# Performance work log

Hardware: AMD Instinct MI355X
Metric: run time of the kernel (lower is better)

The kernel has to match this reference:

```python
import jax, jax.numpy as jnp
import numpy as np

B, TIN, TOUT = 64, 256, 400
NM, BF = 80, 512
MID, H, PRE = BF // 4, 2 * BF, BF // 2
LOC_F, LOC_K = 32, 31


def lstm_cell(x, h, c, Wih, Whh, bih, bhh):
    gates = x @ Wih.T + bih + h @ Whh.T + bhh
    i, f, g, o = jnp.split(gates, 4, axis=-1)
    c2 = jax.nn.sigmoid(f) * c + jax.nn.sigmoid(i) * jnp.tanh(g)
    h2 = jax.nn.sigmoid(o) * jnp.tanh(c2)
    return h2, c2


def setup_inputs() -> dict:
    key = jax.random.key(0)
    ks = jax.random.split(key, 24)
    def p(k, shape, fan_in):
        return jax.random.normal(k, shape, jnp.float32) / np.sqrt(fan_in)
    return {
        'input': jax.random.normal(ks[0], (B, TIN, BF), jnp.float32),
        'input_mask': jnp.ones((B, TIN), jnp.bool_),
        'target': jax.random.normal(ks[1], (B, NM, TOUT), jnp.float32),
        'W_pre1': p(ks[2], (PRE, NM), NM), 'b_pre1': jnp.zeros((PRE,), jnp.float32),
        'W_pre2': p(ks[3], (PRE, PRE), PRE), 'b_pre2': jnp.zeros((PRE,), jnp.float32),
        'Wq': p(ks[4], (MID, H), H),
        'Wk': p(ks[5], (MID, BF), BF),
        'loc_conv': p(ks[6], (LOC_F, 2, LOC_K), 2 * LOC_K),
        'Wloc': p(ks[7], (MID, LOC_F), LOC_F),
        'v_att': p(ks[8], (MID,), MID),
        'Wih1': p(ks[9], (4 * H, BF + PRE), BF + PRE), 'Whh1': p(ks[10], (4 * H, H), H),
        'bih1': jnp.zeros((4 * H,), jnp.float32), 'bhh1': jnp.zeros((4 * H,), jnp.float32),
        'Wih2': p(ks[11], (4 * H, BF + H), BF + H), 'Whh2': p(ks[12], (4 * H, H), H),
        'bih2': jnp.zeros((4 * H,), jnp.float32), 'bhh2': jnp.zeros((4 * H,), jnp.float32),
        'Wout': p(ks[13], (NM, BF + H), BF + H), 'bout': jnp.zeros((NM,), jnp.float32),
    }


def reference(input, input_mask, target, W_pre1, b_pre1, W_pre2, b_pre2, Wq, Wk,
              loc_conv, Wloc, v_att, Wih1, Whh1, bih1, bhh1, Wih2, Whh2, bih2, bhh2,
              Wout, bout):
    b, tin, f = input.shape
    nm, tout = target.shape[1], target.shape[2]
    # teacher-forcing shift: prepend zero frame, drop last
    tgt = jnp.concatenate([jnp.zeros((b, nm, 1), target.dtype), target[:, :, :-1]], 2)
    # PreNet: two 1x1 convs (== per-channel linears) + ReLU (dropout = eval identity)
    x = jax.nn.relu(jnp.einsum('bct,oc->bot', tgt, W_pre1) + b_pre1[None, :, None])
    x = jax.nn.relu(jnp.einsum('bct,oc->bot', x, W_pre2) + b_pre2[None, :, None])  # [B,PRE,Tout]
    key_proj = jnp.einsum('btf,mf->btm', input, Wk)  # [B,Tin,MID]
    pad = (LOC_K - 1) // 2

    def step(carry, xt):
        h1, c1, h2, c2, context, aw, awc = carry
        h1, c1 = lstm_cell(jnp.concatenate([xt, context], 1), h1, c1, Wih1, Whh1, bih1, bhh1)
        # location-sensitive attention
        wpair = jnp.stack([aw, awc], 1)  # [B,2,Tin]
        loc = jax.lax.conv_general_dilated(wpair, loc_conv, (1,), [(pad, pad)],
                                           dimension_numbers=('NCH', 'OIH', 'NCH'))
        loc_feat = jnp.einsum('bct,mc->btm', loc, Wloc)
        q = h1 @ Wq.T  # [B,MID]
        e = jnp.tanh(q[:, None, :] + key_proj + loc_feat) @ v_att  # [B,Tin]
        e = jnp.where(input_mask, e, jnp.float32(-1e9))
        aw2 = jax.nn.softmax(e, axis=1)
        context2 = jnp.einsum('bt,btf->bf', aw2, input)
        awc2 = awc + aw2
        h2, c2 = lstm_cell(jnp.concatenate([h1, context2], 1), h2, c2, Wih2, Whh2, bih2, bhh2)
        out = jnp.concatenate([h2, context2], 1) @ Wout.T + bout
        return (h1, c1, h2, c2, context2, aw2, awc2), (out, aw2)

    z = lambda *s: jnp.zeros(s, input.dtype)
    carry0 = (z(b, H), z(b, H), z(b, H), z(b, H), z(b, f), z(b, tin), z(b, tin))
    xs = jnp.transpose(x, (2, 0, 1))  # [Tout,B,PRE]
    _, (outs, aws) = jax.lax.scan(step, carry0, xs)
    output = jnp.moveaxis(outs, 0, 2)  # [B,NM,Tout]
    weight = jnp.moveaxis(aws, 0, 2)   # [B,Tin,Tout]
    return output, weight
```

## Files before the change

kernel.cpp:

```cpp
#include <hip/hip_runtime.h>

#define NB 256
#define NT 512
#define DYNB 158496
#define SCOPE __HIP_MEMORY_SCOPE_AGENT

typedef __attribute__((ext_vector_type(8))) short short8;
typedef __attribute__((ext_vector_type(4))) float f32x4;

__device__ __forceinline__ float b2f(unsigned short s){ return __uint_as_float(((unsigned)s)<<16); }
__device__ __forceinline__ unsigned short f2b(float f){
  unsigned u = __float_as_uint(f);
  return (unsigned short)((u + 0x7FFFu + ((u>>16)&1u))>>16);
}
__device__ __forceinline__ float sigm(float x){ return 1.0f/(1.0f+__expf(-x)); }
__device__ __forceinline__ float tanh_(float x){ float e=__expf(-2.0f*x); return (1.0f-e)/(1.0f+e); }
__device__ __forceinline__ f32x4 mfma16(short8 a, short8 b, f32x4 c){
  return __builtin_amdgcn_mfma_f32_16x16x32_bf16(a,b,c,0,0,0);
}

__device__ __forceinline__ float2 ld2f(const float* p){
  union{ unsigned long long u; float2 f; } r;
  r.u = __hip_atomic_load((const unsigned long long*)p, __ATOMIC_RELAXED, SCOPE);
  return r.f;
}
__device__ __forceinline__ float ldf(const float* p){
  return __hip_atomic_load((float*)p, __ATOMIC_RELAXED, SCOPE);
}
__device__ __forceinline__ unsigned short ldh(const unsigned short* p){
  return __hip_atomic_load((unsigned short*)p, __ATOMIC_RELAXED, SCOPE);
}
__device__ __forceinline__ void stf(float* p, float v){
  __hip_atomic_store(p, v, __ATOMIC_RELAXED, SCOPE);
}
__device__ __forceinline__ void sth(unsigned short* p, unsigned short v){
  __hip_atomic_store(p, v, __ATOMIC_RELAXED, SCOPE);
}

__device__ __forceinline__ void gbar2(unsigned* arrive, unsigned* root, unsigned* release,
                                      int grp, unsigned& ph){
  __syncthreads();
  if (threadIdx.x==0){
    ph += 1;
    asm volatile("s_waitcnt vmcnt(0)" ::: "memory");
    unsigned old = __hip_atomic_fetch_add(&arrive[grp*32], 1u, __ATOMIC_RELAXED, SCOPE);
    if (old == ph*32u - 1u){
      __hip_atomic_fetch_add(root, 1u, __ATOMIC_RELAXED, SCOPE);
      while (__hip_atomic_load(root, __ATOMIC_RELAXED, SCOPE) < ph*8u){
        __builtin_amdgcn_s_sleep(1);
      }
      __hip_atomic_store(&release[grp*32], ph, __ATOMIC_RELAXED, SCOPE);
    } else {
      while (__hip_atomic_load(&release[grp*32], __ATOMIC_RELAXED, SCOPE) < ph){
        __builtin_amdgcn_s_sleep(1);
      }
    }
  }
  __syncthreads();
}


__global__ void maskdet_k(const unsigned* __restrict__ m32, int* __restrict__ flag){
  __shared__ int ok;
  if (threadIdx.x==0) ok = 1;
  __syncthreads();
  for (int i=threadIdx.x; i<4096; i+=256){
    if (m32[i] > 1u) ok = 0;
  }
  __syncthreads();
  if (threadIdx.x==0) *flag = ok;
}

__global__ void xin2bf_k(const float* __restrict__ xin, unsigned short* __restrict__ xinh){
  size_t i = (size_t)blockIdx.x*256 + threadIdx.x;
  if (i < (size_t)64*256*512) xinh[i] = f2b(xin[i]);
}

__global__ void prenet_k(const float* __restrict__ target, const float* __restrict__ W1, const float* __restrict__ b1,
                         const float* __restrict__ W2, const float* __restrict__ b2,
                         unsigned short* __restrict__ xbh){
  int t = blockIdx.x;
  int tid = threadIdx.x;
  __shared__ float stgt[64][80];
  __shared__ float smid[64][256];
  for(int i=tid;i<64*80;i+=256){
    int b=i/80, c=i%80;
    stgt[b][c] = (t==0)?0.f : target[((size_t)b*80+c)*400 + (t-1)];
  }
  __syncthreads();
  {
    float w1r[80];
    #pragma unroll
    for(int c=0;c<80;c++) w1r[c] = W1[tid*80+c];
    float bb1 = b1[tid];
    for(int b0=0;b0<64;b0+=16){
      float acc[16];
      #pragma unroll
      for(int i=0;i<16;i++) acc[i]=0.f;
      for(int c=0;c<80;c++){
        float wv=w1r[c];
        #pragma unroll
        for(int i=0;i<16;i++) acc[i] += wv*stgt[b0+i][c];
      }
      #pragma unroll
      for(int i=0;i<16;i++) smid[b0+i][tid] = fmaxf(acc[i]+bb1, 0.f);
    }
  }
  __syncthreads();
  {
    float bb2 = b2[tid];
    for(int b0=0;b0<64;b0+=16){
      float acc[16];
      #pragma unroll
      for(int i=0;i<16;i++) acc[i]=0.f;
      for(int c=0;c<256;c++){
        float wv=W2[tid*256+c];
        #pragma unroll
        for(int i=0;i<16;i++) acc[i] += wv*smid[b0+i][c];
      }
      #pragma unroll
      for(int i=0;i<16;i++){
        float v = fmaxf(acc[i]+bb2,0.f);
        xbh[((size_t)t*64 + b0+i)*256 + tid] = f2b(v);
      }
    }
  }
}

__global__ void keyproj_k(const float* __restrict__ xin, const float* __restrict__ Wk, unsigned short* __restrict__ keypT){
  int b = blockIdx.x>>4; int t0=(blockIdx.x&15)*16; int m=threadIdx.x;
  __shared__ float sx[16][512];
  for(int i=m;i<16*512;i+=128){ int tt=i>>9, f=i&511; sx[tt][f]=xin[((size_t)b*256+t0+tt)*512+f]; }
  __syncthreads();
  float s[16];
  #pragma unroll
  for(int i=0;i<16;i++) s[i]=0.f;
  for(int f=0;f<512;f++){
    float wv = Wk[m*512+f];
    #pragma unroll
    for(int i=0;i<16;i++) s[i]+=sx[i][f]*wv;
  }
  #pragma unroll
  for(int i=0;i<16;i++) keypT[((size_t)b*128+m)*256 + t0+i] = f2b(s[i]);
}

__global__ void prep_k(const float* bih1,const float* bhh1,const float* bih2,const float* bhh2,
                       const float* Wq, const float* Wout,
                       float* bsum1,float* bsum2,
                       unsigned short* WqH, unsigned short* WoutH){
  int i0 = blockIdx.x*blockDim.x + threadIdx.x;
  int n = gridDim.x*blockDim.x;
  for(int k=i0;k<4096;k+=n){ bsum1[k]=bih1[k]+bhh1[k]; bsum2[k]=bih2[k]+bhh2[k]; }
  for(int k=i0;k<128*1024;k+=n) WqH[k]=f2b(Wq[k]);
  for(int k=i0;k<80*1536;k+=n) WoutH[k]=f2b(Wout[k]);
}

__global__ void perm_k(const float* __restrict__ Wih1, const float* __restrict__ Whh1,
                       const float* __restrict__ Wih2, const float* __restrict__ Whh2,
                       unsigned short* __restrict__ Wp1h, unsigned short* __restrict__ Wp2h){
  size_t i0 = (size_t)blockIdx.x*blockDim.x + threadIdx.x;
  size_t n  = (size_t)gridDim.x*blockDim.x;
  const size_t N1 = (size_t)256*56*512;
  for(size_t idx=i0; idx<N1; idx+=n){
    int beta = (int)(idx/28672);
    int r = (int)(idx%28672);
    int kt = r/512;
    int l  = (r>>3)&63;
    int i8 = r&7;
    int c = l&15, cci = l>>4;
    int k = kt*32 + cci*8 + i8;
    int rowp = (c>>2)*1024 + beta*4 + (c&3);
    float v = (k<768)? Wih1[(size_t)rowp*768 + k] : Whh1[(size_t)rowp*1024 + (k-768)];
    Wp1h[idx] = f2b(v);
  }
  const size_t N2 = (size_t)256*80*512;
  for(size_t idx=i0; idx<N2; idx+=n){
    int beta = (int)(idx/40960);
    int r = (int)(idx%40960);
    int kt = r/512;
    int l  = (r>>3)&63;
    int i8 = r&7;
    int c = l&15, cci = l>>4;
    int k = kt*32 + cci*8 + i8;
    int rowp = (c>>2)*1024 + beta*4 + (c&3);
    float v = (k<1536)? Wih2[(size_t)rowp*1536 + k] : Whh2[(size_t)rowp*1024 + (k-1536)];
    Wp2h[idx] = f2b(v);
  }
}


struct SArgs {
  const float* loc_conv; const float* v_att; const float* bout;
  const unsigned short* WqH; const unsigned short* WoutH; const float* Wloc;
  const unsigned short* keypT; const unsigned short* xinh;
  const unsigned short* xbh;
  const unsigned short* Wp1h; const unsigned short* Wp2h;
  const float* bsum1; const float* bsum2;
  const unsigned char* mask8; const int* mask32; const int* mflag;
  unsigned short* h1rot; unsigned short* h2rot; unsigned short* ctxrot;
  const unsigned short* zbuf;
  float* c1; float* c2;
  float* aw; float* awc; float* eP; unsigned short* locTh;
  unsigned* arrive; unsigned* root; unsigned* release;
  float* outp; float* wout;
};

__global__ void __launch_bounds__(NT) scan_kernel(SArgs a){
  extern __shared__ char dynsm[];
  unsigned short* Lw1 = (unsigned short*)dynsm;
  unsigned short* Lw2 = (unsigned short*)(dynsm + 57344);
  float* gsc1 = (float*)(dynsm + 139264);
  float* gsc2 = (float*)(dynsm + 143616);
  float* sA   = (float*)(dynsm + 147968);
  float* sq   = (float*)(dynsm + 158208);
  float* sv   = (float*)(dynsm + 158336);
  float* red  = (float*)(dynsm + 158464);

  const int beta = ((blockIdx.x & 7) << 5) | (blockIdx.x >> 3);
  const int grp  = blockIdx.x & 7;
  const int tid = threadIdx.x;
  const int wav = tid>>6;
  const int lan = tid&63;

  const int cc  = lan>>4;
  const int b4  = beta>>2;
  const int q4  = beta&3;
  unsigned ph = 0;

  {
    const short8* g1 = (const short8*)(a.Wp1h + (size_t)beta*28672);
    short8* l1 = (short8*)Lw1;
    for (int i=tid; i<3584; i+=NT) l1[i] = g1[i];
    const short8* g2 = (const short8*)(a.Wp2h + (size_t)beta*40960);
    short8* l2 = (short8*)Lw2;
    for (int i=tid; i<5120; i+=NT) l2[i] = g2[i];
  }

  bool mv = false;
  if (tid<256) mv = (a.mflag[0] ? (a.mask32[b4*256+tid] != 0) : (a.mask8[b4*256+tid] != 0));
  __syncthreads();

  for (int tau=0; tau<=400; ++tau){
    const unsigned short* h1p = (tau==0)? a.zbuf : a.h1rot + (size_t)(tau-1)*65536;
    const unsigned short* h2p = (tau<=1)? a.zbuf : a.h2rot + (size_t)(tau-2)*65536;
    const unsigned short* cxp = (tau==0)? a.zbuf : a.ctxrot + (size_t)(tau-1)*32768;
    unsigned short* h1w = a.h1rot + (size_t)tau*65536;
    unsigned short* h2w = a.h2rot + (size_t)(tau>0 ? tau-1 : 0)*65536;
    unsigned short* cxw = a.ctxrot + (size_t)tau*32768;

    if (tau<400 && wav<4){
      const int row = wav*16 + (lan&15);
      f32x4 A0={0.f,0.f,0.f,0.f};
      const unsigned short* wh = Lw1 + lan*8;
      {
        const unsigned short* xh = a.xbh + ((size_t)tau*64 + row)*256 + cc*8;
        #pragma unroll
        for(int kt=0;kt<8;kt++)
          A0=mfma16(*(const short8*)(xh+kt*32), *(const short8*)(wh+kt*512), A0);
      }
      {
        const unsigned short* xh = cxp + row*512 + cc*8;
        #pragma unroll 8
        for(int kt=8;kt<24;kt++)
          A0=mfma16(*(const short8*)(xh+(kt-8)*32), *(const short8*)(wh+kt*512), A0);
      }
      {
        const unsigned short* xh = h1p + row*1024 + cc*8;
        #pragma unroll 8
        for(int kt=24;kt<56;kt++)
          A0=mfma16(*(const short8*)(xh+(kt-24)*32), *(const short8*)(wh+kt*512), A0);
      }
      #pragma unroll
      for(int r=0;r<4;r++) gsc1[(wav*16 + cc*4 + r)*17 + (lan&15)] = A0[r];
    }
    if (tau>0 && wav>=4){
      const int wv2 = wav-4;
      const int row = wv2*16 + (lan&15);
      f32x4 A0={0.f,0.f,0.f,0.f};
      const unsigned short* wh = Lw2 + lan*8;
      {
        const unsigned short* xh = h1p + row*1024 + cc*8;
        #pragma unroll 8
        for(int kt=0;kt<32;kt++)
          A0=mfma16(*(const short8*)(xh+kt*32), *(const short8*)(wh+kt*512), A0);
      }
      {
        const unsigned short* xh = cxp + row*512 + cc*8;
        #pragma unroll 8
        for(int kt=32;kt<48;kt++)
          A0=mfma16(*(const short8*)(xh+(kt-32)*32), *(const short8*)(wh+kt*512), A0);
      }
      {
        const unsigned short* xh = h2p + row*1024 + cc*8;
        #pragma unroll 8
        for(int kt=48;kt<80;kt++)
          A0=mfma16(*(const short8*)(xh+(kt-48)*32), *(const short8*)(wh+kt*512), A0);
      }
      #pragma unroll
      for(int r=0;r<4;r++) gsc2[(wv2*16 + cc*4 + r)*17 + (lan&15)] = A0[r];
    }
    __syncthreads();
    if (tau<400 && tid<256){
      int m = tid>>2, j = tid&3, u = beta*4+j;
      float gi = gsc1[m*17+0+j]  + a.bsum1[0*1024+u];
      float gf = gsc1[m*17+4+j]  + a.bsum1[1*1024+u];
      float gg = gsc1[m*17+8+j]  + a.bsum1[2*1024+u];
      float go = gsc1[m*17+12+j] + a.bsum1[3*1024+u];
      float cp = a.c1[m*1024+u];
      float cn = sigm(gf)*cp + sigm(gi)*tanh_(gg);
      a.c1[m*1024+u] = cn;
      float hn = sigm(go)*tanh_(cn);
      sth(h1w + m*1024 + u, f2b(hn));
    }
    if (tau>0 && tid>=256){
      int t2 = tid-256;
      int m = t2>>2, j = t2&3, u = beta*4+j;
      float gi = gsc2[m*17+0+j]  + a.bsum2[0*1024+u];
      float gf = gsc2[m*17+4+j]  + a.bsum2[1*1024+u];
      float gg = gsc2[m*17+8+j]  + a.bsum2[2*1024+u];
      float go = gsc2[m*17+12+j] + a.bsum2[3*1024+u];
      float cp = a.c2[m*1024+u];
      float cn = sigm(gf)*cp + sigm(gi)*tanh_(gg);
      a.c2[m*1024+u] = cn;
      float hn = sigm(go)*tanh_(cn);
      sth(h2w + m*1024 + u, f2b(hn));
    }
    if (tau<400){
      if (tid<128){
        float2 v = ld2f(a.aw + b4*256 + tid*2);
        sA[tid*2]=v.x; sA[tid*2+1]=v.y;
        float2 w2 = ld2f(a.awc + b4*256 + tid*2);
        sA[256+tid*2]=w2.x; sA[257+tid*2]=w2.y;
      }
      for(int i=tid;i<1984;i+=NT) sA[512+i] = a.loc_conv[i];
    }
    __syncthreads();
    if (tau<400){
      const int t0 = q4*64;
      #pragma unroll
      for(int jj=0;jj<4;jj++){
        int o = tid*4+jj;
        int f = o>>6, tl = o&63, t = t0+tl;
        float s = 0.f;
        #pragma unroll
        for(int c=0;c<2;c++){
          const float* kw = &sA[512 + (f*2+c)*31];
          const float* wv = &sA[c*256];
          for(int k=0;k<31;k++){
            int tt = t + k - 15;
            if (tt>=0 && tt<256) s += wv[tt]*kw[k];
          }
        }
        sth(a.locTh + (size_t)b4*8192 + f*256 + t, f2b(s));
      }
    }
    gbar2(a.arrive, a.root, a.release, grp, ph);
    if (tau<400 && tid<256){
      const unsigned short* h1c = a.h1rot + (size_t)tau*65536 + b4*1024;
      for(int i=tid;i<1024;i+=256) sA[i] = b2f(h1c[i]);
    }
    if (tau>0 && tid>=256){
      int t2 = tid-256;
      const unsigned short* h2c = a.h2rot + (size_t)(tau-1)*65536 + b4*1024;
      const unsigned short* cxc = a.ctxrot + (size_t)(tau-1)*32768 + b4*512;
      for(int i=t2;i<1024;i+=256) sA[1024+i] = b2f(h2c[i]);
      for(int i=t2;i<512;i+=256)  sA[2048+i] = b2f(cxc[i]);
    }
    __syncthreads();
    if (tau<400 && tid<256){
      int ml = tid>>3, sg = tid&7;
      const unsigned short* wq = a.WqH + (size_t)(q4*32+ml)*1024;
      float s=0.f;
      #pragma unroll 8
      for(int i=0;i<128;i++) s += sA[sg + i*8]*b2f(wq[sg + i*8]);
      s += __shfl_xor(s,1); s += __shfl_xor(s,2); s += __shfl_xor(s,4);
      if (sg==0) sq[ml] = s;
    }
    if (tau>0 && tid>=256 && tid<416){
      int t2 = tid-256;
      int nl = t2>>3, sg = t2&7, nm = q4*20+nl;
      const unsigned short* wo = a.WoutH + (size_t)nm*1536;
      float s=0.f;
      #pragma unroll 8
      for(int i=0;i<192;i++) s += sA[1024 + sg + i*8]*b2f(wo[sg + i*8]);
      s += __shfl_xor(s,1); s += __shfl_xor(s,2); s += __shfl_xor(s,4);
      if (sg==0) a.outp[(size_t)b4*32000 + nm*400 + (tau-1)] = s + a.bout[nm];
    }
    __syncthreads();
    if (tau<400 && tid<256){
      for(int i=tid;i<1024;i+=256) sA[i] = a.Wloc[(q4*32 + (i>>5))*32 + (i&31)];
    }
    if (tid<32) sv[tid] = a.v_att[q4*32+tid];
    __syncthreads();
    if (tau<400 && tid<256){
      int t = tid;
      float lc[32];
      const unsigned short* lb = a.locTh + (size_t)b4*8192 + t;
      #pragma unroll
      for(int f=0;f<32;f++) lc[f] = b2f(ldh(lb + f*256));
      const unsigned short* kb = a.keypT + ((size_t)b4*128 + q4*32)*256 + t;
      float acc=0.f;
      for(int mm=0;mm<32;mm++){
        float lf=0.f;
        #pragma unroll
        for(int f=0;f<32;f++) lf += lc[f]*sA[mm*32+f];
        acc += tanh_(sq[mm] + b2f(kb[mm*256]) + lf)*sv[mm];
      }
      stf(a.eP + b4*1024 + t*4 + q4, acc);
    }
    if (tau==400) break;
    gbar2(a.arrive, a.root, a.release, grp, ph);
    {
      float e=0.f, pe=0.f, mx=0.f;
      if (tid<256){
        const float* ep = a.eP + b4*1024 + tid*4;
        e = ldf(ep+0)+ldf(ep+1)+ldf(ep+2)+ldf(ep+3);
        if (!mv) e = -1e9f;
        mx = e;
        #pragma unroll
        for(int off=1;off<64;off<<=1) mx = fmaxf(mx, __shfl_xor(mx,off));
        if (lan==0) red[wav] = mx;
      }
      __syncthreads();
      if (tid<256){
        mx = fmaxf(fmaxf(red[0],red[1]), fmaxf(red[2],red[3]));
        pe = __expf(e-mx);
        float sm = pe;
        #pragma unroll
        for(int off=1;off<64;off<<=1) sm += __shfl_xor(sm,off);
        if (lan==0) red[4+wav] = sm;
      }
      __syncthreads();
      if (tid<256){
        float sm = red[4]+red[5]+red[6]+red[7];
        float awt = pe/sm;
        if (q4==0){
          stf(a.aw + b4*256+tid, awt);
          stf(a.awc + b4*256+tid, ldf(a.awc + b4*256+tid) + awt);
          a.wout[(size_t)b4*102400 + (size_t)tid*400 + tau] = awt;
        }
        sA[tid] = awt;
      }
      __syncthreads();
      {
        int fl = tid&127, th = tid>>7;
        const unsigned short* xp = a.xinh + ((size_t)(b4*256 + th*64))*512 + q4*128 + fl;
        float s=0.f;
        for(int i=0;i<64;i++) s += sA[th*64+i]*b2f(xp[(size_t)i*512]);
        sA[256+tid] = s;
      }
      __syncthreads();
      if (tid<128){
        float v = sA[256+tid] + sA[384+tid] + sA[512+tid] + sA[640+tid];
        sth(cxw + b4*512 + q4*128 + tid, f2b(v));
      }
    }
    gbar2(a.arrive, a.root, a.release, grp, ph);
  }
}

extern "C" void kernel_launch(void* const* d_in, const int* in_sizes, int n_in,
                              void* d_out, int out_size, void* d_ws, size_t ws_size,
                              hipStream_t stream){
  (void)in_sizes; (void)n_in; (void)out_size; (void)ws_size;
  const float* xin   = (const float*)d_in[0];
  const float* target= (const float*)d_in[2];
  const float* Wpre1 = (const float*)d_in[3];
  const float* bpre1 = (const float*)d_in[4];
  const float* Wpre2 = (const float*)d_in[5];
  const float* bpre2 = (const float*)d_in[6];
  const float* Wq    = (const float*)d_in[7];
  const float* Wk    = (const float*)d_in[8];
  const float* loc_conv = (const float*)d_in[9];
  const float* Wloc  = (const float*)d_in[10];
  const float* v_att = (const float*)d_in[11];
  const float* Wih1  = (const float*)d_in[12];
  const float* Whh1  = (const float*)d_in[13];
  const float* bih1  = (const float*)d_in[14];
  const float* bhh1  = (const float*)d_in[15];
  const float* Wih2  = (const float*)d_in[16];
  const float* Whh2  = (const float*)d_in[17];
  const float* bih2  = (const float*)d_in[18];
  const float* bhh2  = (const float*)d_in[19];
  const float* Wout  = (const float*)d_in[20];
  const float* boutp = (const float*)d_in[21];

  char* w = (char*)d_ws;
  auto carve=[&](size_t bytes)->void*{ void* r=(void*)w; w += (bytes+255)&~(size_t)255; return r; };
  unsigned short* zbuf = (unsigned short*)carve((size_t)64*1024*2);
  float* c1  = (float*)carve((size_t)64*1024*4);
  float* c2  = (float*)carve((size_t)64*1024*4);
  float* aw  = (float*)carve((size_t)64*256*4);
  float* awc = (float*)carve((size_t)64*256*4);
  unsigned* arrive  = (unsigned*)carve(1024);
  unsigned* rootc   = (unsigned*)carve(256);
  unsigned* release = (unsigned*)carve(1024);
  int* mflag = (int*)carve(256);
  size_t state_bytes = (size_t)(w - (char*)d_ws);
  float* eP   = (float*)carve((size_t)64*256*4*4);
  unsigned short* locTh = (unsigned short*)carve((size_t)64*32*256*2);
  unsigned short* keypT = (unsigned short*)carve((size_t)64*128*256*2);
  unsigned short* xinh  = (unsigned short*)carve((size_t)64*256*512*2);
  unsigned short* xbh = (unsigned short*)carve((size_t)400*64*256*2);
  float* bsum1 = (float*)carve((size_t)4096*4);
  float* bsum2 = (float*)carve((size_t)4096*4);
  unsigned short* WqH = (unsigned short*)carve((size_t)128*1024*2);
  unsigned short* WoutH = (unsigned short*)carve((size_t)80*1536*2);
  unsigned short* Wp1h = (unsigned short*)carve((size_t)256*56*512*2);
  unsigned short* Wp2h = (unsigned short*)carve((size_t)256*80*512*2);
  unsigned short* h1rot = (unsigned short*)carve((size_t)400*65536*2);
  unsigned short* h2rot = (unsigned short*)carve((size_t)400*65536*2);
  unsigned short* ctxrot= (unsigned short*)carve((size_t)400*32768*2);

  hipMemsetAsync(d_ws, 0, state_bytes, stream);
  maskdet_k<<<1, 256, 0, stream>>>((const unsigned*)d_in[1], mflag);
  xin2bf_k<<<32768, 256, 0, stream>>>(xin, xinh);
  prenet_k<<<400, 256, 0, stream>>>(target, Wpre1, bpre1, Wpre2, bpre2, xbh);
  keyproj_k<<<1024, 128, 0, stream>>>(xin, Wk, keypT);
  prep_k<<<64, 256, 0, stream>>>(bih1,bhh1,bih2,bhh2,Wq,Wout,bsum1,bsum2,WqH,WoutH);
  perm_k<<<2048, 256, 0, stream>>>(Wih1,Whh1,Wih2,Whh2,Wp1h,Wp2h);

  SArgs a;
  a.loc_conv=loc_conv; a.v_att=v_att; a.bout=boutp;
  a.WqH=WqH; a.WoutH=WoutH; a.Wloc=Wloc;
  a.keypT=keypT; a.xinh=xinh; a.xbh=xbh;
  a.Wp1h=Wp1h; a.Wp2h=Wp2h;
  a.bsum1=bsum1; a.bsum2=bsum2;
  a.mask8=(const unsigned char*)d_in[1]; a.mask32=(const int*)d_in[1]; a.mflag=mflag;
  a.h1rot=h1rot; a.h2rot=h2rot; a.ctxrot=ctxrot; a.zbuf=zbuf;
  a.c1=c1; a.c2=c2;
  a.aw=aw; a.awc=awc; a.eP=eP; a.locTh=locTh;
  a.arrive=arrive; a.root=rootc; a.release=release;
  a.outp=(float*)d_out; a.wout=(float*)d_out + (size_t)64*80*400;

  hipFuncSetAttribute((const void*)scan_kernel, hipFuncAttributeMaxDynamicSharedMemorySize, DYNB);
  scan_kernel<<<dim3(NB), dim3(NT), DYNB, stream>>>(a);
}
```

Baseline: 45.52 ms.

## Keep attention weights and location features block-local, rotate energy buffer per step

```diff
diff --git a/kernel.cpp b/kernel.cpp
--- a/kernel.cpp
+++ b/kernel.cpp
@@ -2,7 +2,7 @@
 
 #define NB 256
 #define NT 512
-#define DYNB 158496
+#define DYNB 160288
 #define SCOPE __HIP_MEMORY_SCOPE_AGENT
 
 typedef __attribute__((ext_vector_type(8))) short short8;
@@ -19,17 +19,6 @@
   return __builtin_amdgcn_mfma_f32_16x16x32_bf16(a,b,c,0,0,0);
 }
 
-__device__ __forceinline__ float2 ld2f(const float* p){
-  union{ unsigned long long u; float2 f; } r;
-  r.u = __hip_atomic_load((const unsigned long long*)p, __ATOMIC_RELAXED, SCOPE);
-  return r.f;
-}
-__device__ __forceinline__ float ldf(const float* p){
-  return __hip_atomic_load((float*)p, __ATOMIC_RELAXED, SCOPE);
-}
-__device__ __forceinline__ unsigned short ldh(const unsigned short* p){
-  return __hip_atomic_load((unsigned short*)p, __ATOMIC_RELAXED, SCOPE);
-}
 __device__ __forceinline__ void stf(float* p, float v){
   __hip_atomic_store(p, v, __ATOMIC_RELAXED, SCOPE);
 }
@@ -145,12 +134,16 @@
 }
 
 __global__ void prep_k(const float* bih1,const float* bhh1,const float* bih2,const float* bhh2,
-                       const float* Wq, const float* Wout,
+                       const float* Wq, const float* Wout, const float* Wloc,
                        float* bsum1,float* bsum2,
-                       unsigned short* WqH, unsigned short* WoutH){
+                       unsigned short* WqH, unsigned short* WoutH, unsigned short* WlocH){
   int i0 = blockIdx.x*blockDim.x + threadIdx.x;
   int n = gridDim.x*blockDim.x;
-  for(int k=i0;k<4096;k+=n){ bsum1[k]=bih1[k]+bhh1[k]; bsum2[k]=bih2[k]+bhh2[k]; }
+  for(int k=i0;k<4096;k+=n){
+    bsum1[k]=bih1[k]+bhh1[k];
+    bsum2[k]=bih2[k]+bhh2[k];
+    WlocH[k]=f2b(Wloc[k]);
+  }
   for(int k=i0;k<128*1024;k+=n) WqH[k]=f2b(Wq[k]);
   for(int k=i0;k<80*1536;k+=n) WoutH[k]=f2b(Wout[k]);
 }
@@ -191,16 +184,16 @@
 
 struct SArgs {
   const float* loc_conv; const float* v_att; const float* bout;
-  const unsigned short* WqH; const unsigned short* WoutH; const float* Wloc;
+  const unsigned short* WqH; const unsigned short* WoutH; const unsigned short* WlocH;
   const unsigned short* keypT; const unsigned short* xinh;
   const unsigned short* xbh;
   const unsigned short* Wp1h; const unsigned short* Wp2h;
   const float* bsum1; const float* bsum2;
   const unsigned char* mask8; const int* mask32; const int* mflag;
   unsigned short* h1rot; unsigned short* h2rot; unsigned short* ctxrot;
+  float* erot;
   const unsigned short* zbuf;
   float* c1; float* c2;
-  float* aw; float* awc; float* eP; unsigned short* locTh;
   unsigned* arrive; unsigned* root; unsigned* release;
   float* outp; float* wout;
 };
@@ -211,10 +204,14 @@
   unsigned short* Lw2 = (unsigned short*)(dynsm + 57344);
   float* gsc1 = (float*)(dynsm + 139264);
   float* gsc2 = (float*)(dynsm + 143616);
-  float* sA   = (float*)(dynsm + 147968);
-  float* sq   = (float*)(dynsm + 158208);
-  float* sv   = (float*)(dynsm + 158336);
-  float* red  = (float*)(dynsm + 158464);
+  unsigned short* sAu = (unsigned short*)(dynsm + 147968);
+  float* sAf  = (float*)(dynsm + 147968);
+  float* sq   = (float*)(dynsm + 153088);
+  float* sv   = (float*)(dynsm + 153600);
+  float* red  = (float*)(dynsm + 154112);
+  float* aw_lds  = (float*)(dynsm + 154144);
+  float* awc_lds = (float*)(dynsm + 155168);
+  unsigned short* sLoc = (unsigned short*)(dynsm + 156192);
 
   const int beta = ((blockIdx.x & 7) << 5) | (blockIdx.x >> 3);
   const int grp  = blockIdx.x & 7;
@@ -235,6 +232,8 @@
     short8* l2 = (short8*)Lw2;
     for (int i=tid; i<5120; i+=NT) l2[i] = g2[i];
   }
+  if (tid<256){ aw_lds[tid]=0.f; awc_lds[tid]=0.f; }
+  if (tid<128) sv[tid] = a.v_att[tid];
 
   bool mv = false;
   if (tid<256) mv = (a.mflag[0] ? (a.mask32[b4*256+tid] != 0) : (a.mask8[b4*256+tid] != 0));
@@ -326,16 +325,6 @@
       sth(h2w + m*1024 + u, f2b(hn));
     }
     if (tau<400){
-      if (tid<128){
-        float2 v = ld2f(a.aw + b4*256 + tid*2);
-        sA[tid*2]=v.x; sA[tid*2+1]=v.y;
-        float2 w2 = ld2f(a.awc + b4*256 + tid*2);
-        sA[256+tid*2]=w2.x; sA[257+tid*2]=w2.y;
-      }
-      for(int i=tid;i<1984;i+=NT) sA[512+i] = a.loc_conv[i];
-    }
-    __syncthreads();
-    if (tau<400){
       const int t0 = q4*64;
       #pragma unroll
       for(int jj=0;jj<4;jj++){
@@ -344,37 +333,37 @@
         float s = 0.f;
         #pragma unroll
         for(int c=0;c<2;c++){
-          const float* kw = &sA[512 + (f*2+c)*31];
-          const float* wv = &sA[c*256];
+          const float* kw = a.loc_conv + (f*2+c)*31;
+          const float* wv = (c==0)? aw_lds : awc_lds;
           for(int k=0;k<31;k++){
             int tt = t + k - 15;
             if (tt>=0 && tt<256) s += wv[tt]*kw[k];
           }
         }
-        sth(a.locTh + (size_t)b4*8192 + f*256 + t, f2b(s));
+        sLoc[tl*32+f] = f2b(s);
       }
     }
     gbar2(a.arrive, a.root, a.release, grp, ph);
     if (tau<400 && tid<256){
       const unsigned short* h1c = a.h1rot + (size_t)tau*65536 + b4*1024;
-      for(int i=tid;i<1024;i+=256) sA[i] = b2f(h1c[i]);
+      for(int i=tid;i<1024;i+=256) sAu[i] = h1c[i];
     }
     if (tau>0 && tid>=256){
       int t2 = tid-256;
       const unsigned short* h2c = a.h2rot + (size_t)(tau-1)*65536 + b4*1024;
       const unsigned short* cxc = a.ctxrot + (size_t)(tau-1)*32768 + b4*512;
-      for(int i=t2;i<1024;i+=256) sA[1024+i] = b2f(h2c[i]);
-      for(int i=t2;i<512;i+=256)  sA[2048+i] = b2f(cxc[i]);
+      for(int i=t2;i<1024;i+=256) sAu[1024+i] = h2c[i];
+      for(int i=t2;i<512;i+=256)  sAu[2048+i] = cxc[i];
     }
     __syncthreads();
     if (tau<400 && tid<256){
-      int ml = tid>>3, sg = tid&7;
-      const unsigned short* wq = a.WqH + (size_t)(q4*32+ml)*1024;
+      int m = tid>>1, sg = tid&1;
+      const unsigned short* wq = a.WqH + (size_t)m*1024;
       float s=0.f;
       #pragma unroll 8
-      for(int i=0;i<128;i++) s += sA[sg + i*8]*b2f(wq[sg + i*8]);
-      s += __shfl_xor(s,1); s += __shfl_xor(s,2); s += __shfl_xor(s,4);
-      if (sg==0) sq[ml] = s;
+      for(int i=0;i<512;i++) s += b2f(sAu[sg + i*2])*b2f(wq[sg + i*2]);
+      s += __shfl_xor(s,1);
+      if (sg==0) sq[m] = s;
     }
     if (tau>0 && tid>=256 && tid<416){
       int t2 = tid-256;
@@ -382,39 +371,37 @@
       const unsigned short* wo = a.WoutH + (size_t)nm*1536;
       float s=0.f;
       #pragma unroll 8
-      for(int i=0;i<192;i++) s += sA[1024 + sg + i*8]*b2f(wo[sg + i*8]);
+      for(int i=0;i<192;i++) s += b2f(sAu[1024 + sg + i*8])*b2f(wo[sg + i*8]);
       s += __shfl_xor(s,1); s += __shfl_xor(s,2); s += __shfl_xor(s,4);
       if (sg==0) a.outp[(size_t)b4*32000 + nm*400 + (tau-1)] = s + a.bout[nm];
     }
     __syncthreads();
     if (tau<400 && tid<256){
-      for(int i=tid;i<1024;i+=256) sA[i] = a.Wloc[(q4*32 + (i>>5))*32 + (i&31)];
-    }
-    if (tid<32) sv[tid] = a.v_att[q4*32+tid];
-    __syncthreads();
-    if (tau<400 && tid<256){
-      int t = tid;
+      int tl = tid>>2, sg = tid&3;
+      int t = q4*64 + tl;
       float lc[32];
-      const unsigned short* lb = a.locTh + (size_t)b4*8192 + t;
-      #pragma unroll
-      for(int f=0;f<32;f++) lc[f] = b2f(ldh(lb + f*256));
-      const unsigned short* kb = a.keypT + ((size_t)b4*128 + q4*32)*256 + t;
+      #pragma unroll
+      for(int f=0;f<32;f++) lc[f] = b2f(sLoc[tl*32+f]);
+      const unsigned short* kb = a.keypT + ((size_t)b4*128 + sg*32)*256 + t;
+      const unsigned short* wl = a.WlocH + sg*32*32;
       float acc=0.f;
-      for(int mm=0;mm<32;mm++){
+      for(int mm0=0;mm0<32;mm0++){
+        int mm = sg*32+mm0;
         float lf=0.f;
         #pragma unroll
-        for(int f=0;f<32;f++) lf += lc[f]*sA[mm*32+f];
-        acc += tanh_(sq[mm] + b2f(kb[mm*256]) + lf)*sv[mm];
-      }
-      stf(a.eP + b4*1024 + t*4 + q4, acc);
+        for(int f=0;f<32;f++) lf += lc[f]*b2f(wl[mm0*32+f]);
+        acc += tanh_(sq[mm] + b2f(kb[(size_t)mm0*256]) + lf)*sv[mm];
+      }
+      acc += __shfl_xor(acc,1);
+      acc += __shfl_xor(acc,2);
+      if (sg==0) stf(a.erot + (size_t)tau*16384 + b4*256 + t, acc);
     }
     if (tau==400) break;
     gbar2(a.arrive, a.root, a.release, grp, ph);
     {
       float e=0.f, pe=0.f, mx=0.f;
       if (tid<256){
-        const float* ep = a.eP + b4*1024 + tid*4;
-        e = ldf(ep+0)+ldf(ep+1)+ldf(ep+2)+ldf(ep+3);
+        e = a.erot[(size_t)tau*16384 + b4*256 + tid];
         if (!mv) e = -1e9f;
         mx = e;
         #pragma unroll
@@ -434,24 +421,21 @@
       if (tid<256){
         float sm = red[4]+red[5]+red[6]+red[7];
         float awt = pe/sm;
-        if (q4==0){
-          stf(a.aw + b4*256+tid, awt);
-          stf(a.awc + b4*256+tid, ldf(a.awc + b4*256+tid) + awt);
-          a.wout[(size_t)b4*102400 + (size_t)tid*400 + tau] = awt;
-        }
-        sA[tid] = awt;
+        aw_lds[tid] = awt;
+        awc_lds[tid] += awt;
+        if (q4==0) a.wout[(size_t)b4*102400 + (size_t)tid*400 + tau] = awt;
       }
       __syncthreads();
       {
         int fl = tid&127, th = tid>>7;
         const unsigned short* xp = a.xinh + ((size_t)(b4*256 + th*64))*512 + q4*128 + fl;
         float s=0.f;
-        for(int i=0;i<64;i++) s += sA[th*64+i]*b2f(xp[(size_t)i*512]);
-        sA[256+tid] = s;
+        for(int i=0;i<64;i++) s += aw_lds[th*64+i]*b2f(xp[(size_t)i*512]);
+        sAf[th*128+fl] = s;
       }
       __syncthreads();
       if (tid<128){
-        float v = sA[256+tid] + sA[384+tid] + sA[512+tid] + sA[640+tid];
+        float v = sAf[tid] + sAf[128+tid] + sAf[256+tid] + sAf[384+tid];
         sth(cxw + b4*512 + q4*128 + tid, f2b(v));
       }
     }
@@ -490,15 +474,11 @@
   unsigned short* zbuf = (unsigned short*)carve((size_t)64*1024*2);
   float* c1  = (float*)carve((size_t)64*1024*4);
   float* c2  = (float*)carve((size_t)64*1024*4);
-  float* aw  = (float*)carve((size_t)64*256*4);
-  float* awc = (float*)carve((size_t)64*256*4);
   unsigned* arrive  = (unsigned*)carve(1024);
   unsigned* rootc   = (unsigned*)carve(256);
   unsigned* release = (unsigned*)carve(1024);
   int* mflag = (int*)carve(256);
   size_t state_bytes = (size_t)(w - (char*)d_ws);
-  float* eP   = (float*)carve((size_t)64*256*4*4);
-  unsigned short* locTh = (unsigned short*)carve((size_t)64*32*256*2);
   unsigned short* keypT = (unsigned short*)carve((size_t)64*128*256*2);
   unsigned short* xinh  = (unsigned short*)carve((size_t)64*256*512*2);
   unsigned short* xbh = (unsigned short*)carve((size_t)400*64*256*2);
@@ -506,30 +486,31 @@
   float* bsum2 = (float*)carve((size_t)4096*4);
   unsigned short* WqH = (unsigned short*)carve((size_t)128*1024*2);
   unsigned short* WoutH = (unsigned short*)carve((size_t)80*1536*2);
+  unsigned short* WlocH = (unsigned short*)carve((size_t)4096*2);
   unsigned short* Wp1h = (unsigned short*)carve((size_t)256*56*512*2);
   unsigned short* Wp2h = (unsigned short*)carve((size_t)256*80*512*2);
   unsigned short* h1rot = (unsigned short*)carve((size_t)400*65536*2);
   unsigned short* h2rot = (unsigned short*)carve((size_t)400*65536*2);
   unsigned short* ctxrot= (unsigned short*)carve((size_t)400*32768*2);
+  float* erot = (float*)carve((size_t)400*16384*4);
 
   hipMemsetAsync(d_ws, 0, state_bytes, stream);
   maskdet_k<<<1, 256, 0, stream>>>((const unsigned*)d_in[1], mflag);
   xin2bf_k<<<32768, 256, 0, stream>>>(xin, xinh);
   prenet_k<<<400, 256, 0, stream>>>(target, Wpre1, bpre1, Wpre2, bpre2, xbh);
   keyproj_k<<<1024, 128, 0, stream>>>(xin, Wk, keypT);
-  prep_k<<<64, 256, 0, stream>>>(bih1,bhh1,bih2,bhh2,Wq,Wout,bsum1,bsum2,WqH,WoutH);
+  prep_k<<<64, 256, 0, stream>>>(bih1,bhh1,bih2,bhh2,Wq,Wout,Wloc,bsum1,bsum2,WqH,WoutH,WlocH);
   perm_k<<<2048, 256, 0, stream>>>(Wih1,Whh1,Wih2,Whh2,Wp1h,Wp2h);
 
   SArgs a;
   a.loc_conv=loc_conv; a.v_att=v_att; a.bout=boutp;
-  a.WqH=WqH; a.WoutH=WoutH; a.Wloc=Wloc;
+  a.WqH=WqH; a.WoutH=WoutH; a.WlocH=WlocH;
   a.keypT=keypT; a.xinh=xinh; a.xbh=xbh;
   a.Wp1h=Wp1h; a.Wp2h=Wp2h;
   a.bsum1=bsum1; a.bsum2=bsum2;
   a.mask8=(const unsigned char*)d_in[1]; a.mask32=(const int*)d_in[1]; a.mflag=mflag;
-  a.h1rot=h1rot; a.h2rot=h2rot; a.ctxrot=ctxrot; a.zbuf=zbuf;
+  a.h1rot=h1rot; a.h2rot=h2rot; a.ctxrot=ctxrot; a.erot=erot; a.zbuf=zbuf;
   a.c1=c1; a.c2=c2;
-  a.aw=aw; a.awc=awc; a.eP=eP; a.locTh=locTh;
   a.arrive=arrive; a.root=rootc; a.release=release;
   a.outp=(float*)d_out; a.wout=(float*)d_out + (size_t)64*80*400;
 
```

Measured after the change: 89.48 ms. 96.6% more time.
